# Kernel tuning notes

Hardware: AMD Instinct MI355X
Metric: run time of the kernel (lower is better)

## Reference

```python
import jax, jax.numpy as jnp
import numpy as np
from jax import lax

N, L, D = 8, 2048, 512
KS = [3, 5]
DECAY = 0.2


def setup_inputs() -> dict:
    key = jax.random.key(0)
    k1, k2, k3, k4, k5 = jax.random.split(key, 5)
    return {
        "qa_embed_data": jax.random.normal(k1, (N, L, D), dtype=jnp.float32),
        "conv_w3": jax.random.normal(k2, (D, 1, KS[0]), dtype=jnp.float32) * (1.0 / KS[0]),
        "conv_w5": jax.random.normal(k3, (D, 1, KS[1]), dtype=jnp.float32) * (1.0 / KS[1]),
        "fusion_w": jax.random.normal(k4, (D, 2 * D), dtype=jnp.float32) * 0.02,
        "fusion_b": jax.random.normal(k5, (D,), dtype=jnp.float32) * 0.02,
    }


def causal_depthwise_conv(x, w, k):
    # x: [N, L, C], w: [C, 1, k] (depthwise, groups=C). Left-pad by k-1 (causal).
    xc = jnp.transpose(x, (0, 2, 1))  # [N, C, L]
    y = lax.conv_general_dilated(
        xc, w, window_strides=(1,), padding=[(k - 1, 0)],
        feature_group_count=x.shape[-1],
        dimension_numbers=("NCH", "OIH", "NCH"))
    return jnp.transpose(y, (0, 2, 1))  # [N, L, C]


def squash(v):
    norm = jnp.linalg.norm(v, axis=-1, keepdims=True)
    scale = norm ** 2 / (1.0 + norm ** 2)
    return scale * v / (norm + 1e-9)


def dynamic_routing(u, num_iterations):
    # u: [N, L, M, C]
    n, l, m, _ = u.shape
    logits = jnp.zeros((n, l, m), dtype=u.dtype)
    v = None
    for i in range(num_iterations):
        c = jax.nn.softmax(logits, axis=-1)
        s = jnp.einsum("nlm,nlmc->nlc", c, u)
        v = squash(s)
        if i < num_iterations - 1:
            logits = logits + jnp.einsum("nlmc,nlc->nlm", u, v)
    return v


def time_attention(x):
    # x: [N, L, C]; causal attention with exp(-decay*dist) bias -> add -decay*dist in log space
    l = x.shape[1]
    sim = jnp.einsum("nlc,nmc->nlm", x, x)  # [N, L, L]
    idx = jnp.arange(l)
    dist = (idx[:, None] - idx[None, :]).astype(x.dtype)  # query - key
    mask = dist >= 0  # lower-triangular causal mask
    ws = jnp.where(mask[None], sim - DECAY * dist[None], -jnp.inf)
    attn = jax.nn.softmax(ws, axis=-1)
    return jnp.einsum("nlm,nmc->nlc", attn, x)


def reference(qa_embed_data, conv_w3, conv_w5, fusion_w, fusion_b):
    trend3 = causal_depthwise_conv(qa_embed_data, conv_w3, KS[0])
    trend5 = causal_depthwise_conv(qa_embed_data, conv_w5, KS[1])
    seasonal = jnp.stack([qa_embed_data - trend3, qa_embed_data - trend5], axis=2)  # [N,L,2,C]
    trend = jnp.stack([trend3, trend5], axis=2)  # [N,L,2,C]
    seasonal_f = time_attention(dynamic_routing(seasonal, 3))
    trend_f = time_attention(dynamic_routing(trend, 3))
    cat = jnp.concatenate([seasonal_f, trend_f], axis=-1)  # [N,L,2C]
    return cat @ fusion_w.T + fusion_b
```

## Files before the change

kernel.cpp:

```cpp
#include <hip/hip_runtime.h>


typedef short     bf16x8 __attribute__((ext_vector_type(8)));
typedef float     f32x4  __attribute__((ext_vector_type(4)));
typedef unsigned short u16;
typedef u16       u16x8  __attribute__((ext_vector_type(8)));
typedef u16       u16x4  __attribute__((ext_vector_type(4)));

#define NBATCH 8
#define LSEQ   2048
#define DCH    512
#define DPAD   520
#define TPAD   524
#define DECAYF 0.2f
#define WTILES 4

typedef const __attribute__((address_space(1))) unsigned char* gas_t;
typedef __attribute__((address_space(3))) unsigned char* las_t;
__device__ __forceinline__ void dma16(const void* g, void* l) {
    __builtin_amdgcn_global_load_lds((gas_t)g, (las_t)l, 16, 0, 0);
}

__device__ __forceinline__ u16 f2bf(float f) {
    unsigned int u = __float_as_uint(f);
    u += 0x7fffu + ((u >> 16) & 1u);
    return (u16)(u >> 16);
}

__device__ __forceinline__ void wave_sum6(float& a, float& b, float& c,
                                          float& d, float& e, float& f) {
#pragma unroll
    for (int m = 1; m < 64; m <<= 1) {
        float ta = __shfl_xor(a, m, 64);
        float tb = __shfl_xor(b, m, 64);
        float tc = __shfl_xor(c, m, 64);
        float td = __shfl_xor(d, m, 64);
        float te = __shfl_xor(e, m, 64);
        float tf = __shfl_xor(f, m, 64);
        a += ta; b += tb; c += tc; d += td; e += te; f += tf;
    }
}

__global__ __launch_bounds__(512) void conv_route(
    const float* __restrict__ x, const float* __restrict__ w3, const float* __restrict__ w5,
    u16* __restrict__ vs, u16* __restrict__ vt,
    u16* __restrict__ vsTt, u16* __restrict__ vtTt)
{
    __shared__ u16 Ts[2][32][TPAD];

    const int tid  = threadIdx.x;
    const int wid  = tid >> 6, lane = tid & 63;
    const int pb   = blockIdx.x * 32 + wid * 4;
    const int n    = pb >> 11;
    const int l0   = pb & (LSEQ - 1);
    const int c0   = lane * 8;

    float f3[24], f5[40];
#pragma unroll
    for (int k = 0; k < 6; ++k)  ((float4*)f3)[k] = ((const float4*)(w3 + (size_t)c0*3))[k];
#pragma unroll
    for (int k = 0; k < 10; ++k) ((float4*)f5)[k] = ((const float4*)(w5 + (size_t)c0*5))[k];

    float xm[5][8];
#pragma unroll
    for (int j = 0; j < 5; ++j) {
        int ll = l0 - j;
        if (ll >= 0) {
            const float4* sp = (const float4*)(x + ((size_t)(n*LSEQ + ll))*DCH + c0);
            float4 a = sp[0], b = sp[1];
            xm[j][0]=a.x; xm[j][1]=a.y; xm[j][2]=a.z; xm[j][3]=a.w;
            xm[j][4]=b.x; xm[j][5]=b.y; xm[j][6]=b.z; xm[j][7]=b.w;
        } else {
#pragma unroll
            for (int i = 0; i < 8; ++i) xm[j][i] = 0.f;
        }
    }

#pragma unroll
    for (int s = 0; s < 4; ++s) {
        const int l = l0 + s;
        if (s > 0) {
#pragma unroll
            for (int j = 4; j > 0; --j)
#pragma unroll
                for (int i = 0; i < 8; ++i) xm[j][i] = xm[j-1][i];
            const float4* sp = (const float4*)(x + ((size_t)(n*LSEQ + l))*DCH + c0);
            float4 a = sp[0], b = sp[1];
            xm[0][0]=a.x; xm[0][1]=a.y; xm[0][2]=a.z; xm[0][3]=a.w;
            xm[0][4]=b.x; xm[0][5]=b.y; xm[0][6]=b.z; xm[0][7]=b.w;
        }

        float t3[8], t5[8], a0[8], a1[8];
#pragma unroll
        for (int i = 0; i < 8; ++i) {
            t3[i] = f3[i*3+0]*xm[2][i] + f3[i*3+1]*xm[1][i] + f3[i*3+2]*xm[0][i];
            t5[i] = f5[i*5+0]*xm[4][i] + f5[i*5+1]*xm[3][i] + f5[i*5+2]*xm[2][i]
                  + f5[i*5+3]*xm[1][i] + f5[i*5+4]*xm[0][i];
            a0[i] = xm[0][i] - t3[i];
            a1[i] = xm[0][i] - t5[i];
        }

        float A1=0.f, B1=0.f, C1=0.f, A2=0.f, B2=0.f, C2=0.f;
#pragma unroll
        for (int i = 0; i < 8; ++i) {
            A1 += a0[i]*a0[i]; B1 += a0[i]*a1[i]; C1 += a1[i]*a1[i];
            A2 += t3[i]*t3[i]; B2 += t3[i]*t5[i]; C2 += t5[i]*t5[i];
        }
        wave_sum6(A1, B1, C1, A2, B2, C2);

        float ba0=0.f, ba1=0.f, bb0=0.f, bb1=0.f;
        float ca0=0.5f, ca1=0.5f, sca=0.f, cb0=0.5f, cb1=0.5f, scb=0.f;
#pragma unroll
        for (int it = 0; it < 3; ++it) {
            float mxa = fmaxf(ba0, ba1), mxb = fmaxf(bb0, bb1);
            float ea0 = __expf(ba0-mxa), ea1 = __expf(ba1-mxa);
            float eb0 = __expf(bb0-mxb), eb1 = __expf(bb1-mxb);
            float ia = 1.f/(ea0+ea1), ib = 1.f/(eb0+eb1);
            ca0 = ea0*ia; ca1 = ea1*ia; cb0 = eb0*ib; cb1 = eb1*ib;
            float na = ca0*ca0*A1 + 2.f*ca0*ca1*B1 + ca1*ca1*C1;
            float nb = cb0*cb0*A2 + 2.f*cb0*cb1*B2 + cb1*cb1*C2;
            sca = na / ((1.f + na) * (sqrtf(na) + 1e-9f));
            scb = nb / ((1.f + nb) * (sqrtf(nb) + 1e-9f));
            if (it < 2) {
                ba0 += sca*(ca0*A1 + ca1*B1);
                ba1 += sca*(ca0*B1 + ca1*C1);
                bb0 += scb*(cb0*A2 + cb1*B2);
                bb1 += scb*(cb0*B2 + cb1*C2);
            }
        }

        u16x8 pa, pb8;
#pragma unroll
        for (int i = 0; i < 8; ++i) {
            pa[i]  = f2bf(sca*(ca0*a0[i] + ca1*a1[i]));
            pb8[i] = f2bf(scb*(cb0*t3[i] + cb1*t5[i]));
        }
        *(u16x8*)(vs + (size_t)(pb + s)*DPAD + c0) = pa;
        *(u16x8*)(vt + (size_t)(pb + s)*DPAD + c0) = pb8;
        *(u16x8*)(&Ts[0][wid*4 + s][c0]) = pa;
        *(u16x8*)(&Ts[1][wid*4 + s][c0]) = pb8;
    }
    __syncthreads();

#pragma unroll
    for (int k = 0; k < 8; ++k) {
        int id = k*512 + tid;
        int z = id >> 11, rem = id & 2047, ch = rem >> 2, so = rem & 3;
        u16x8 o;
#pragma unroll
        for (int j = 0; j < 8; ++j) {
            int s = so*8 + j;
            int key = (s >> 1) + ((s & 1) << 4);
            o[j] = Ts[z][key][ch];
        }
        u16* dst = (z ? vtTt : vsTt) + (size_t)blockIdx.x * (DCH*32);
        *(u16x8*)(dst + ch*32 + so*8) = o;
    }
}

__global__ __launch_bounds__(256) void attn(
    const u16* __restrict__ vs, const u16* __restrict__ vt,
    const u16* __restrict__ vsTt, const u16* __restrict__ vtTt,
    u16* __restrict__ cat)
{
    __shared__ u16 Ks[33792/2];
    __shared__ u16 Vs[DCH*32];
    __shared__ unsigned int Ps32[4][16][20];

    const int inst = blockIdx.y;
    const int t = inst >> 3, n = inst & 7;
    const u16* src  = (t ? vt : vs) + (size_t)n * LSEQ * DPAD;
    const u16* srcT = (t ? vtTt : vsTt) + (size_t)n * 64 * DCH * 32;

    const int bx = blockIdx.x;
    const int r0 = (((bx & 7) << 2) | (bx >> 3)) * 64;

    const int tid  = threadIdx.x;
    const int wid  = tid >> 6, lane = tid & 63;
    const int l16  = lane & 15, quad = lane >> 4;

    bf16x8 qf[16];
    {
        const u16* qp = src + (size_t)(r0 + wid*16 + l16) * DPAD + quad*8;
#pragma unroll
        for (int kc = 0; kc < 16; ++kc) qf[kc] = *(const bf16x8*)(qp + kc*32);
    }

    f32x4 O[32];
#pragma unroll
    for (int i = 0; i < 32; ++i) O[i] = (f32x4){0.f, 0.f, 0.f, 0.f};
    f32x4 O2 = {0.f, 0.f, 0.f, 0.f};

    bf16x8 ones8;
#pragma unroll
    for (int i = 0; i < 8; ++i) ones8[i] = (short)0x3F80;

    const int kb_hi = (r0 >> 5) + 1;
    const int kb_lo = (kb_hi >= WTILES) ? kb_hi - (WTILES-1) : 0;

    {
        const u16* gK = src + (size_t)kb_lo * 32 * DPAD;
        for (int i = wid; i < 33; i += 4) dma16(gK + i*512 + lane*8, Ks + i*512);
    }

    for (int kb = kb_lo; kb <= kb_hi; ++kb) {
        __syncthreads();
        {
            const u16* gV = srcT + (size_t)kb * (DCH*32);
            for (int i = wid; i < 32; i += 4) dma16(gV + i*512 + lane*8, Vs + i*512);
        }

        f32x4 S0a = {0.f,0.f,0.f,0.f}, S1a = {0.f,0.f,0.f,0.f};
        f32x4 S0b = {0.f,0.f,0.f,0.f}, S1b = {0.f,0.f,0.f,0.f};
#pragma unroll
        for (int kc = 0; kc < 8; ++kc) {
            bf16x8 b0 = *(const bf16x8*)(Ks + (size_t)l16*DPAD + kc*32 + quad*8);
            bf16x8 b1 = *(const bf16x8*)(Ks + (size_t)(16+l16)*DPAD + kc*32 + quad*8);
            S0a = __builtin_amdgcn_mfma_f32_16x16x32_bf16(qf[kc], b0, S0a, 0, 0, 0);
            S1a = __builtin_amdgcn_mfma_f32_16x16x32_bf16(qf[kc], b1, S1a, 0, 0, 0);
        }
#pragma unroll
        for (int kc = 8; kc < 16; ++kc) {
            bf16x8 b0 = *(const bf16x8*)(Ks + (size_t)l16*DPAD + kc*32 + quad*8);
            bf16x8 b1 = *(const bf16x8*)(Ks + (size_t)(16+l16)*DPAD + kc*32 + quad*8);
            S0b = __builtin_amdgcn_mfma_f32_16x16x32_bf16(qf[kc], b0, S0b, 0, 0, 0);
            S1b = __builtin_amdgcn_mfma_f32_16x16x32_bf16(qf[kc], b1, S1b, 0, 0, 0);
        }
        f32x4 S0 = S0a + S0b, S1 = S1a + S1b;

        const int rowg = r0 + wid*16 + quad*4;
#pragma unroll
        for (int r = 0; r < 4; ++r) {
            int row = rowg + r;
            int d0  = row - (kb*32 + l16);
            int d1  = d0 - 16;
            float p0 = (d0 >= 0) ? __expf(fmaf(-DECAYF, (float)d0, S0[r] - 1.f)) : 0.f;
            float p1 = (d1 >= 0) ? __expf(fmaf(-DECAYF, (float)d1, S1[r] - 1.f)) : 0.f;
            Ps32[wid][quad*4 + r][l16] = ((unsigned)f2bf(p1) << 16) | (unsigned)f2bf(p0);
        }

        __syncthreads();
        if (kb < kb_hi) {
            const u16* gK = src + (size_t)(kb+1) * 32 * DPAD;
            for (int i = wid; i < 33; i += 4) dma16(gK + i*512 + lane*8, Ks + i*512);
        }

        bf16x8 pf = *(const bf16x8*)(&Ps32[wid][l16][quad*4]);
#pragma unroll
        for (int ct = 0; ct < 32; ++ct) {
            bf16x8 vf = *(const bf16x8*)(Vs + (size_t)(ct*16 + l16)*32 + quad*8);
            O[ct] = __builtin_amdgcn_mfma_f32_16x16x32_bf16(pf, vf, O[ct], 0, 0, 0);
        }
        O2 = __builtin_amdgcn_mfma_f32_16x16x32_bf16(pf, ones8, O2, 0, 0, 0);
    }

    float inv[4];
#pragma unroll
    for (int r = 0; r < 4; ++r) inv[r] = 1.f / O2[r];
    const size_t rowbase = (size_t)n * LSEQ + r0 + wid*16 + quad*4;
    const int colbase = t * 512 + l16;
#pragma unroll
    for (int ct = 0; ct < 32; ++ct) {
#pragma unroll
        for (int r = 0; r < 4; ++r)
            cat[(rowbase + r) * 1024 + colbase + ct*16] = f2bf(O[ct][r] * inv[r]);
    }
}

__global__ __launch_bounds__(256) void cast_w(const float* __restrict__ w, u16* __restrict__ wb)
{
    int id = blockIdx.x * 256 + threadIdx.x;
    float4 f = ((const float4*)w)[id];
    u16x4 o;
    o[0] = f2bf(f.x); o[1] = f2bf(f.y); o[2] = f2bf(f.z); o[3] = f2bf(f.w);
    ((u16x4*)wb)[id] = o;
}

__global__ __launch_bounds__(256) void fusion_gemm(
    const u16* __restrict__ A, const u16* __restrict__ Wb,
    const float* __restrict__ bias, float* __restrict__ out)
{
    __shared__ u16 As[64*64];
    __shared__ u16 Bs[128*64];
    const int m0 = blockIdx.x * 64;
    const int n0 = blockIdx.y * 128;
    const int tid = threadIdx.x;
    const int wid = tid >> 6, lane = tid & 63;
    const int l16 = lane & 15, quad = lane >> 4;

    f32x4 acc[4][2];
#pragma unroll
    for (int i = 0; i < 4; ++i)
#pragma unroll
        for (int j = 0; j < 2; ++j) acc[i][j] = (f32x4){0.f, 0.f, 0.f, 0.f};

    for (int kb = 0; kb < 16; ++kb) {
        __syncthreads();
#pragma unroll
        for (int i = 0; i < 2; ++i) {
            int q = i*256 + tid, r = q >> 3, kp = q & 7;
            int kl = kp ^ (r & 7);
            dma16(A + (size_t)(m0 + r)*1024 + kb*64 + kl*8, As + q*8);
        }
#pragma unroll
        for (int i = 0; i < 4; ++i) {
            int q = i*256 + tid, r = q >> 3, kp = q & 7;
            int kl = kp ^ (r & 7);
            dma16(Wb + (size_t)(n0 + r)*1024 + kb*64 + kl*8, Bs + q*8);
        }
        __syncthreads();
#pragma unroll
        for (int k2 = 0; k2 < 2; ++k2) {
            const int kl = k2*4 + quad;
            bf16x8 af[4], bf2[2];
#pragma unroll
            for (int i = 0; i < 4; ++i) {
                int r = i*16 + l16;
                af[i] = *(const bf16x8*)(As + r*64 + (kl ^ (r & 7))*8);
            }
#pragma unroll
            for (int j = 0; j < 2; ++j) {
                int r = wid*32 + j*16 + l16;
                bf2[j] = *(const bf16x8*)(Bs + r*64 + (kl ^ (r & 7))*8);
            }
#pragma unroll
            for (int i = 0; i < 4; ++i)
#pragma unroll
                for (int j = 0; j < 2; ++j)
                    acc[i][j] = __builtin_amdgcn_mfma_f32_16x16x32_bf16(af[i], bf2[j], acc[i][j], 0, 0, 0);
        }
    }
#pragma unroll
    for (int j = 0; j < 2; ++j) {
        int col = n0 + wid*32 + j*16 + l16;
        float bv = bias[col];
#pragma unroll
        for (int i = 0; i < 4; ++i) {
            int rowb = m0 + i*16 + quad*4;
#pragma unroll
            for (int r = 0; r < 4; ++r)
                out[(size_t)(rowb + r)*512 + col] = acc[i][j][r] + bv;
        }
    }
}

extern "C" void kernel_launch(void* const* d_in, const int* in_sizes, int n_in,
                              void* d_out, int out_size, void* d_ws, size_t ws_size,
                              hipStream_t stream)
{
    (void)in_sizes; (void)n_in; (void)out_size; (void)ws_size;
    const float* x  = (const float*)d_in[0];
    const float* w3 = (const float*)d_in[1];
    const float* w5 = (const float*)d_in[2];
    const float* fw = (const float*)d_in[3];
    const float* fb = (const float*)d_in[4];
    float* out = (float*)d_out;

    const size_t SZP = (size_t)NBATCH * LSEQ * DPAD;
    const size_t SZT = (size_t)NBATCH * 64 * DCH * 32;
    u16* vs   = (u16*)d_ws;
    u16* vt   = vs   + SZP;
    u16* vsTt = vt   + SZP;
    u16* vtTt = vsTt + SZT;
    u16* cat  = vtTt + SZT;
    u16* wb   = cat  + (size_t)NBATCH*LSEQ*1024;

    cast_w     <<<512, 256, 0, stream>>>(fw, wb);
    conv_route <<<512, 512, 0, stream>>>(x, w3, w5, vs, vt, vsTt, vtTt);
    attn       <<<dim3(32, 16), 256, 0, stream>>>(vs, vt, vsTt, vtTt, cat);
    fusion_gemm<<<dim3(256, 4), 256, 0, stream>>>(cat, wb, fb, out);
}
```

Before: 171.2 us.

## Build transposed V tile in LDS from K tile instead of precomputed global copy

The conv_route kernel no longer writes transposed V copies to global memory. It now handles one position per wave with many more blocks and drops the LDS transpose stage. Inside attention, each key tile already in LDS is transposed into a padded V buffer, so the separate V DMA stream is gone. This removes global write and read traffic, but adds LDS transpose work with strided 16-bit reads inside the attention loop, and it is unclear whether the existing barriers order that work safely against the next K DMA.

```diff
diff --git a/kernel.cpp b/kernel.cpp
--- a/kernel.cpp
+++ b/kernel.cpp
@@ -11,7 +11,7 @@
 #define LSEQ   2048
 #define DCH    512
 #define DPAD   520
-#define TPAD   524
+#define VSTR   40
 #define DECAYF 0.2f
 #define WTILES 4
 
@@ -41,30 +41,20 @@
     }
 }
 
-__global__ __launch_bounds__(512) void conv_route(
+__global__ __launch_bounds__(256) void conv_route(
     const float* __restrict__ x, const float* __restrict__ w3, const float* __restrict__ w5,
-    u16* __restrict__ vs, u16* __restrict__ vt,
-    u16* __restrict__ vsTt, u16* __restrict__ vtTt)
-{
-    __shared__ u16 Ts[2][32][TPAD];
-
-    const int tid  = threadIdx.x;
-    const int wid  = tid >> 6, lane = tid & 63;
-    const int pb   = blockIdx.x * 32 + wid * 4;
-    const int n    = pb >> 11;
-    const int l0   = pb & (LSEQ - 1);
-    const int c0   = lane * 8;
-
-    float f3[24], f5[40];
-#pragma unroll
-    for (int k = 0; k < 6; ++k)  ((float4*)f3)[k] = ((const float4*)(w3 + (size_t)c0*3))[k];
-#pragma unroll
-    for (int k = 0; k < 10; ++k) ((float4*)f5)[k] = ((const float4*)(w5 + (size_t)c0*5))[k];
+    u16* __restrict__ vs, u16* __restrict__ vt)
+{
+    const int wid  = threadIdx.x >> 6;
+    const int lane = threadIdx.x & 63;
+    const int p = blockIdx.x * 4 + wid;
+    const int n = p >> 11, l = p & (LSEQ - 1);
+    const int c0 = lane * 8;
 
     float xm[5][8];
 #pragma unroll
     for (int j = 0; j < 5; ++j) {
-        int ll = l0 - j;
+        int ll = l - j;
         if (ll >= 0) {
             const float4* sp = (const float4*)(x + ((size_t)(n*LSEQ + ll))*DCH + c0);
             float4 a = sp[0], b = sp[1];
@@ -75,102 +65,71 @@
             for (int i = 0; i < 8; ++i) xm[j][i] = 0.f;
         }
     }
-
-#pragma unroll
-    for (int s = 0; s < 4; ++s) {
-        const int l = l0 + s;
-        if (s > 0) {
-#pragma unroll
-            for (int j = 4; j > 0; --j)
-#pragma unroll
-                for (int i = 0; i < 8; ++i) xm[j][i] = xm[j-1][i];
-            const float4* sp = (const float4*)(x + ((size_t)(n*LSEQ + l))*DCH + c0);
-            float4 a = sp[0], b = sp[1];
-            xm[0][0]=a.x; xm[0][1]=a.y; xm[0][2]=a.z; xm[0][3]=a.w;
-            xm[0][4]=b.x; xm[0][5]=b.y; xm[0][6]=b.z; xm[0][7]=b.w;
-        }
-
-        float t3[8], t5[8], a0[8], a1[8];
-#pragma unroll
-        for (int i = 0; i < 8; ++i) {
-            t3[i] = f3[i*3+0]*xm[2][i] + f3[i*3+1]*xm[1][i] + f3[i*3+2]*xm[0][i];
-            t5[i] = f5[i*5+0]*xm[4][i] + f5[i*5+1]*xm[3][i] + f5[i*5+2]*xm[2][i]
-                  + f5[i*5+3]*xm[1][i] + f5[i*5+4]*xm[0][i];
-            a0[i] = xm[0][i] - t3[i];
-            a1[i] = xm[0][i] - t5[i];
-        }
-
-        float A1=0.f, B1=0.f, C1=0.f, A2=0.f, B2=0.f, C2=0.f;
-#pragma unroll
-        for (int i = 0; i < 8; ++i) {
-            A1 += a0[i]*a0[i]; B1 += a0[i]*a1[i]; C1 += a1[i]*a1[i];
-            A2 += t3[i]*t3[i]; B2 += t3[i]*t5[i]; C2 += t5[i]*t5[i];
-        }
-        wave_sum6(A1, B1, C1, A2, B2, C2);
-
-        float ba0=0.f, ba1=0.f, bb0=0.f, bb1=0.f;
-        float ca0=0.5f, ca1=0.5f, sca=0.f, cb0=0.5f, cb1=0.5f, scb=0.f;
-#pragma unroll
-        for (int it = 0; it < 3; ++it) {
-            float mxa = fmaxf(ba0, ba1), mxb = fmaxf(bb0, bb1);
-            float ea0 = __expf(ba0-mxa), ea1 = __expf(ba1-mxa);
-            float eb0 = __expf(bb0-mxb), eb1 = __expf(bb1-mxb);
-            float ia = 1.f/(ea0+ea1), ib = 1.f/(eb0+eb1);
-            ca0 = ea0*ia; ca1 = ea1*ia; cb0 = eb0*ib; cb1 = eb1*ib;
-            float na = ca0*ca0*A1 + 2.f*ca0*ca1*B1 + ca1*ca1*C1;
-            float nb = cb0*cb0*A2 + 2.f*cb0*cb1*B2 + cb1*cb1*C2;
-            sca = na / ((1.f + na) * (sqrtf(na) + 1e-9f));
-            scb = nb / ((1.f + nb) * (sqrtf(nb) + 1e-9f));
-            if (it < 2) {
-                ba0 += sca*(ca0*A1 + ca1*B1);
-                ba1 += sca*(ca0*B1 + ca1*C1);
-                bb0 += scb*(cb0*A2 + cb1*B2);
-                bb1 += scb*(cb0*B2 + cb1*C2);
-            }
-        }
-
-        u16x8 pa, pb8;
-#pragma unroll
-        for (int i = 0; i < 8; ++i) {
-            pa[i]  = f2bf(sca*(ca0*a0[i] + ca1*a1[i]));
-            pb8[i] = f2bf(scb*(cb0*t3[i] + cb1*t5[i]));
-        }
-        *(u16x8*)(vs + (size_t)(pb + s)*DPAD + c0) = pa;
-        *(u16x8*)(vt + (size_t)(pb + s)*DPAD + c0) = pb8;
-        *(u16x8*)(&Ts[0][wid*4 + s][c0]) = pa;
-        *(u16x8*)(&Ts[1][wid*4 + s][c0]) = pb8;
-    }
-    __syncthreads();
-
-#pragma unroll
-    for (int k = 0; k < 8; ++k) {
-        int id = k*512 + tid;
-        int z = id >> 11, rem = id & 2047, ch = rem >> 2, so = rem & 3;
-        u16x8 o;
-#pragma unroll
-        for (int j = 0; j < 8; ++j) {
-            int s = so*8 + j;
-            int key = (s >> 1) + ((s & 1) << 4);
-            o[j] = Ts[z][key][ch];
-        }
-        u16* dst = (z ? vtTt : vsTt) + (size_t)blockIdx.x * (DCH*32);
-        *(u16x8*)(dst + ch*32 + so*8) = o;
-    }
+    float f3[24], f5[40];
+#pragma unroll
+    for (int k = 0; k < 6; ++k)  ((float4*)f3)[k] = ((const float4*)(w3 + (size_t)c0*3))[k];
+#pragma unroll
+    for (int k = 0; k < 10; ++k) ((float4*)f5)[k] = ((const float4*)(w5 + (size_t)c0*5))[k];
+
+    float t3[8], t5[8], a0[8], a1[8];
+#pragma unroll
+    for (int i = 0; i < 8; ++i) {
+        t3[i] = f3[i*3+0]*xm[2][i] + f3[i*3+1]*xm[1][i] + f3[i*3+2]*xm[0][i];
+        t5[i] = f5[i*5+0]*xm[4][i] + f5[i*5+1]*xm[3][i] + f5[i*5+2]*xm[2][i]
+              + f5[i*5+3]*xm[1][i] + f5[i*5+4]*xm[0][i];
+        a0[i] = xm[0][i] - t3[i];
+        a1[i] = xm[0][i] - t5[i];
+    }
+
+    float A1=0.f, B1=0.f, C1=0.f, A2=0.f, B2=0.f, C2=0.f;
+#pragma unroll
+    for (int i = 0; i < 8; ++i) {
+        A1 += a0[i]*a0[i]; B1 += a0[i]*a1[i]; C1 += a1[i]*a1[i];
+        A2 += t3[i]*t3[i]; B2 += t3[i]*t5[i]; C2 += t5[i]*t5[i];
+    }
+    wave_sum6(A1, B1, C1, A2, B2, C2);
+
+    float ba0=0.f, ba1=0.f, bb0=0.f, bb1=0.f;
+    float ca0=0.5f, ca1=0.5f, sca=0.f, cb0=0.5f, cb1=0.5f, scb=0.f;
+#pragma unroll
+    for (int it = 0; it < 3; ++it) {
+        float mxa = fmaxf(ba0, ba1), mxb = fmaxf(bb0, bb1);
+        float ea0 = __expf(ba0-mxa), ea1 = __expf(ba1-mxa);
+        float eb0 = __expf(bb0-mxb), eb1 = __expf(bb1-mxb);
+        float ia = 1.f/(ea0+ea1), ib = 1.f/(eb0+eb1);
+        ca0 = ea0*ia; ca1 = ea1*ia; cb0 = eb0*ib; cb1 = eb1*ib;
+        float na = ca0*ca0*A1 + 2.f*ca0*ca1*B1 + ca1*ca1*C1;
+        float nb = cb0*cb0*A2 + 2.f*cb0*cb1*B2 + cb1*cb1*C2;
+        sca = na / ((1.f + na) * (sqrtf(na) + 1e-9f));
+        scb = nb / ((1.f + nb) * (sqrtf(nb) + 1e-9f));
+        if (it < 2) {
+            ba0 += sca*(ca0*A1 + ca1*B1);
+            ba1 += sca*(ca0*B1 + ca1*C1);
+            bb0 += scb*(cb0*A2 + cb1*B2);
+            bb1 += scb*(cb0*B2 + cb1*C2);
+        }
+    }
+    u16x8 pa, pb;
+#pragma unroll
+    for (int i = 0; i < 8; ++i) {
+        pa[i] = f2bf(sca*(ca0*a0[i] + ca1*a1[i]));
+        pb[i] = f2bf(scb*(cb0*t3[i] + cb1*t5[i]));
+    }
+    *(u16x8*)(vs + (size_t)p*DPAD + c0) = pa;
+    *(u16x8*)(vt + (size_t)p*DPAD + c0) = pb;
 }
 
 __global__ __launch_bounds__(256) void attn(
     const u16* __restrict__ vs, const u16* __restrict__ vt,
-    const u16* __restrict__ vsTt, const u16* __restrict__ vtTt,
     u16* __restrict__ cat)
 {
     __shared__ u16 Ks[33792/2];
-    __shared__ u16 Vs[DCH*32];
+    __shared__ u16 Vs[DCH*VSTR];
     __shared__ unsigned int Ps32[4][16][20];
 
     const int inst = blockIdx.y;
     const int t = inst >> 3, n = inst & 7;
-    const u16* src  = (t ? vt : vs) + (size_t)n * LSEQ * DPAD;
-    const u16* srcT = (t ? vtTt : vsTt) + (size_t)n * 64 * DCH * 32;
+    const u16* src = (t ? vt : vs) + (size_t)n * LSEQ * DPAD;
 
     const int bx = blockIdx.x;
     const int r0 = (((bx & 7) << 2) | (bx >> 3)) * 64;
@@ -205,10 +164,6 @@
 
     for (int kb = kb_lo; kb <= kb_hi; ++kb) {
         __syncthreads();
-        {
-            const u16* gV = srcT + (size_t)kb * (DCH*32);
-            for (int i = wid; i < 32; i += 4) dma16(gV + i*512 + lane*8, Vs + i*512);
-        }
 
         f32x4 S0a = {0.f,0.f,0.f,0.f}, S1a = {0.f,0.f,0.f,0.f};
         f32x4 S0b = {0.f,0.f,0.f,0.f}, S1b = {0.f,0.f,0.f,0.f};
@@ -227,6 +182,21 @@
             S1b = __builtin_amdgcn_mfma_f32_16x16x32_bf16(qf[kc], b1, S1b, 0, 0, 0);
         }
         f32x4 S0 = S0a + S0b, S1 = S1a + S1b;
+
+#pragma unroll
+        for (int pass = 0; pass < 2; ++pass) {
+            const int ch = pass*256 + tid;
+#pragma unroll
+            for (int g = 0; g < 4; ++g) {
+                u16x8 o;
+#pragma unroll
+                for (int j = 0; j < 4; ++j) {
+                    o[2*j]   = Ks[(size_t)(g*4 + j)      * DPAD + ch];
+                    o[2*j+1] = Ks[(size_t)(g*4 + j + 16) * DPAD + ch];
+                }
+                *(u16x8*)(Vs + ch*VSTR + g*8) = o;
+            }
+        }
 
         const int rowg = r0 + wid*16 + quad*4;
 #pragma unroll
@@ -248,7 +218,7 @@
         bf16x8 pf = *(const bf16x8*)(&Ps32[wid][l16][quad*4]);
 #pragma unroll
         for (int ct = 0; ct < 32; ++ct) {
-            bf16x8 vf = *(const bf16x8*)(Vs + (size_t)(ct*16 + l16)*32 + quad*8);
+            bf16x8 vf = *(const bf16x8*)(Vs + (size_t)(ct*16 + l16)*VSTR + quad*8);
             O[ct] = __builtin_amdgcn_mfma_f32_16x16x32_bf16(pf, vf, O[ct], 0, 0, 0);
         }
         O2 = __builtin_amdgcn_mfma_f32_16x16x32_bf16(pf, ones8, O2, 0, 0, 0);
@@ -357,16 +327,13 @@
     float* out = (float*)d_out;
 
     const size_t SZP = (size_t)NBATCH * LSEQ * DPAD;
-    const size_t SZT = (size_t)NBATCH * 64 * DCH * 32;
     u16* vs   = (u16*)d_ws;
     u16* vt   = vs   + SZP;
-    u16* vsTt = vt   + SZP;
-    u16* vtTt = vsTt + SZT;
-    u16* cat  = vtTt + SZT;
+    u16* cat  = vt   + SZP;
     u16* wb   = cat  + (size_t)NBATCH*LSEQ*1024;
 
     cast_w     <<<512, 256, 0, stream>>>(fw, wb);
-    conv_route <<<512, 512, 0, stream>>>(x, w3, w5, vs, vt, vsTt, vtTt);
-    attn       <<<dim3(32, 16), 256, 0, stream>>>(vs, vt, vsTt, vtTt, cat);
+    conv_route <<<4096, 256, 0, stream>>>(x, w3, w5, vs, vt);
+    attn       <<<dim3(32, 16), 256, 0, stream>>>(vs, vt, cat);
     fusion_gemm<<<dim3(256, 4), 256, 0, stream>>>(cat, wb, fb, out);
 }
```

Result: faster. 166.9 us (-2.5%).
